# Kernel tuning notes

Measured on AMD Instinct MI355X. Metric: run time of the kernel, lower is better.

The kernel has to match this reference:

```python
import jax, jax.numpy as jnp
import numpy as np

PATCH = 16
FMAP = 14  # 224 // 16, feature-map / mask resolution
BLUR_K = np.array([[1., 2., 1.], [2., 4., 2.], [1., 2., 1.]], dtype=np.float32) / 16.0  # pascal(3), normalized


def _conv(x, w, stride, pad):
    return jax.lax.conv_general_dilated(
        x, w, (stride, stride), [(pad, pad), (pad, pad)],
        dimension_numbers=("NCHW", "OIHW", "NCHW"))


def _max_blur_pool(x):
    # MaxBlurPool2D(kernel_size=3, stride=2, max_pool_size=2, ceil_mode=False):
    x = jax.lax.reduce_window(x, -jnp.inf, jax.lax.max,
                              (1, 1, 2, 2), (1, 1, 1, 1), "VALID")
    C = x.shape[1]
    kw = jnp.broadcast_to(jnp.asarray(BLUR_K, x.dtype), (C, 1, 3, 3))
    return jax.lax.conv_general_dilated(
        x, kw, (2, 2), [(1, 1), (1, 1)],
        dimension_numbers=("NCHW", "OIHW", "NCHW"), feature_group_count=C)


def _up(m, hw):
    # upsample [B,1,FMAP,FMAP] mask to spatial size hw via repeat_interleave
    f = hw // FMAP
    return jnp.repeat(jnp.repeat(m, f, axis=2), f, axis=3)


def reference(x, masks, w1, w2):
    B = x.shape[0]
    m = masks.reshape(B, 1, FMAP, FMAP).astype(x.dtype)  # fmap-level active mask
    x = x * _up(m, x.shape[2])                 # _apply_masks: zero masked 16x16 patches
    x = _conv(x, w1, 2, 3)                     # B,64,112,112
    x = jax.nn.relu(x * _up(m, x.shape[2]))    # SparK-style sparse conv: re-mask output
    x = _max_blur_pool(x)                      # B,64,56,56
    x = _conv(x, w2, 2, 3)                     # B,768,28,28
    x = jax.nn.relu(x * _up(m, x.shape[2]))    # re-mask output of second sparse conv
    x = _max_blur_pool(x)                      # B,768,14,14
    B_, C, H, W = x.shape
    return x.reshape(B_, C, H * W).transpose(0, 2, 1)  # b (h w) c -> [B,196,768]


def setup_inputs() -> dict:
    key = jax.random.key(0)
    k1, k2, k3, k4 = jax.random.split(key, 4)
    x = jax.random.normal(k1, (64, 3, 224, 224), jnp.float32)
    masks = jax.random.randint(k2, (64, 196), 0, 2).astype(bool)
    # kaiming_normal fan_in scaling as in init_weight
    w1 = jax.random.normal(k3, (64, 3, 7, 7), jnp.float32) * np.float32(np.sqrt(2.0 / (3 * 49)))
    w2 = jax.random.normal(k4, (768, 64, 7, 7), jnp.float32) * np.float32(np.sqrt(2.0 / (64 * 49)))
    return {"x": x, "masks": masks, "w1": w1, "w2": w2}
```

## Files before the change

### kernel.cpp

```cpp
#include <hip/hip_runtime.h>
#include <stdint.h>

typedef __attribute__((ext_vector_type(8))) short short8;
typedef __attribute__((ext_vector_type(4))) float f32x4;

#define DEVFN static __device__ __forceinline__

DEVFN float bf2f(uint16_t u) { union { uint32_t i; float f; } v; v.i = ((uint32_t)u) << 16; return v.f; }
DEVFN uint16_t f2bf(float f) {
  union { float f; uint32_t i; } v; v.f = f;
  uint32_t u = v.i;
  u += 0x7fffu + ((u >> 16) & 1u);
  return (uint16_t)(u >> 16);
}
DEVFN int imin(int a, int b) { return a < b ? a : b; }

DEVFN void gl_lds16(const void* g, void* l) {
  __builtin_amdgcn_global_load_lds(
      (__attribute__((address_space(1))) void*)(void*)g,
      (__attribute__((address_space(3))) void*)l, 16, 0, 0);
}

DEVFN f32x4 mfma16(short8 a, short8 b, f32x4 c) {
  return __builtin_amdgcn_mfma_f32_16x16x32_bf16(a, b, c, 0, 0, 0);
}

static constexpr size_t OFF_XP   = 0;
static constexpr size_t OFF_W1T  = 27557888;
static constexpr size_t OFF_W2T  = 27586560;
static constexpr size_t OFF_Y1   = 32403456;
static constexpr size_t OFF_P1   = 135163904;
static constexpr size_t OFF_Y2   = 166653952;
static constexpr size_t OFF_LIST = 243724288;
static constexpr size_t OFF_CNT  = 243774464;
static constexpr size_t WS_NEED  = 243774664;

__global__ __launch_bounds__(256) void k_count(const int* __restrict__ masks, int* __restrict__ cnts) {
  int b = blockIdx.x;
  int gid = b * 256 + threadIdx.x;
  unsigned long long m = __ballot(masks[gid] != 0);
  __shared__ int wsum[4];
  if ((threadIdx.x & 63) == 0) wsum[threadIdx.x >> 6] = __popcll(m);
  __syncthreads();
  if (threadIdx.x == 0) cnts[b] = wsum[0] + wsum[1] + wsum[2] + wsum[3];
}

__global__ __launch_bounds__(256) void k_emit(const int* __restrict__ masks, const int* __restrict__ cnts,
                                              int* __restrict__ list, int* __restrict__ total) {
  int b = blockIdx.x;
  int gid = b * 256 + threadIdx.x;
  int lane = threadIdx.x & 63, wave = threadIdx.x >> 6;
  int base = 0;
  for (int i = 0; i < b; ++i) base += cnts[i];
  bool f = masks[gid] != 0;
  unsigned long long m = __ballot(f);
  __shared__ int wcnt[4];
  if (lane == 0) wcnt[wave] = __popcll(m);
  __syncthreads();
  int woff = 0;
  for (int i = 0; i < wave; ++i) woff += wcnt[i];
  if (f) list[base + woff + __popcll(m & ((1ull << lane) - 1ull))] = gid;
  if (b == 48 && threadIdx.x == 0)
    *total = base + wcnt[0] + wcnt[1] + wcnt[2] + wcnt[3];
}

__global__ __launch_bounds__(256) void k_prep(const float* __restrict__ x, const int* __restrict__ masks,
                                              uint16_t* __restrict__ xp) {
  int gid = blockIdx.x * 256 + threadIdx.x;
  int b = gid / 53824;
  int rc = gid - b * 53824;
  int r2 = rc / 232;
  int c2 = rc - r2 * 232;
  int r = r2 - 3, c = c2 - 3;
  uint16_t o0 = 0, o1 = 0, o2 = 0;
  if ((unsigned)r < 224u && (unsigned)c < 224u) {
    if (masks[b * 196 + (r >> 4) * 14 + (c >> 4)]) {
      const float* px = x + (((size_t)b * 3) * 224 + r) * 224 + c;
      o0 = f2bf(px[0]);
      o1 = f2bf(px[50176]);
      o2 = f2bf(px[100352]);
    }
  }
  ushort4 o; o.x = o0; o.y = o1; o.z = o2; o.w = 0;
  *(ushort4*)(xp + (size_t)gid * 4) = o;
}

__global__ __launch_bounds__(256) void k_wt(const float* __restrict__ w1, const float* __restrict__ w2,
                                            uint16_t* __restrict__ w1t, uint16_t* __restrict__ w2t) {
  int gid = blockIdx.x * 256 + threadIdx.x;
  if (gid < 14336) {
    int kh = gid / 2048; int r = gid - kh * 2048;
    int oc = r >> 5, slot = r & 31;
    int kw = slot >> 2, ic = slot & 3;
    float v = 0.f;
    if (kw < 7 && ic < 3) v = w1[((oc * 3 + ic) * 7 + kh) * 7 + kw];
    w1t[gid] = f2bf(v);
  } else {
    int g2 = gid - 14336;
    int khw = g2 / 49152; int r = g2 - khw * 49152;
    int oc = r >> 6, ic = r & 63;
    int kh = khw / 7, kw = khw - kh * 7;
    w2t[g2] = f2bf(w2[((oc * 64 + ic) * 7 + kh) * 7 + kw]);
  }
}

__global__ __launch_bounds__(256, 3) void k_conv1(const uint16_t* __restrict__ xp, const uint16_t* __restrict__ w1t,
                                                  const int* __restrict__ list, const int* __restrict__ count,
                                                  uint16_t* __restrict__ y1) {
  __shared__ uint16_t sB[7 * 64 * 32];
  __shared__ int sc[2];

  int cnt = *count;
  int blk = blockIdx.x;
  if (blk * 2 >= cnt) return;
  int tid = threadIdx.x, lane = tid & 63, wave = tid >> 6;
  int csw = (lane & 3) ^ ((lane >> 2) & 3);

  {
    const char* wg = (const char*)w1t;
    char* wl = (char*)sB;
#pragma unroll
    for (int t = 0; t < 7; ++t) {
      int ldsoff = t * 4096 + wave * 1024;
      int goff = t * 4096 + (wave * 16 + (lane >> 2)) * 64 + csw * 16;
      gl_lds16(wg + goff, wl + ldsoff);
    }
  }
  if (tid < 2) sc[tid] = list[imin(blk * 2 + tid, cnt - 1)];
  __syncthreads();

  int wm = wave * 32, mrow = lane & 15, kg = lane >> 4;

  const uint16_t* baseA[2];
#pragma unroll
  for (int i = 0; i < 2; ++i) {
    int row = wm + 16 * i + mrow;
    int cell = sc[row >> 6];
    int b = cell / 196, cc = cell - b * 196;
    int ci = cc / 14, cj = cc - ci * 14;
    int p = row & 63;
    int oh = ci * 8 + (p >> 3), ow = cj * 8 + (p & 7);
    baseA[i] = xp + (((size_t)(b * 232 + 2 * oh)) * 232 + 2 * ow) * 4 + kg * 8;
  }
  int ksw = (kg ^ (mrow & 3)) * 8;

  f32x4 acc[2][4];
#pragma unroll
  for (int i = 0; i < 2; ++i)
#pragma unroll
    for (int j = 0; j < 4; ++j) acc[i][j] = f32x4{0.f, 0.f, 0.f, 0.f};

#pragma unroll
  for (int kh = 0; kh < 7; ++kh) {
    short8 a0 = *(const short8*)(baseA[0] + kh * 928);
    short8 a1 = *(const short8*)(baseA[1] + kh * 928);
    const uint16_t* Bk = sB + kh * 2048;
#pragma unroll
    for (int j = 0; j < 4; ++j) {
      short8 bj = *(const short8*)(Bk + (16 * j + mrow) * 32 + ksw);
      acc[0][j] = mfma16(a0, bj, acc[0][j]);
      acc[1][j] = mfma16(a1, bj, acc[1][j]);
    }
  }

#pragma unroll
  for (int i = 0; i < 2; ++i) {
    int rbase = wm + 16 * i;
    int cellidx = blk * 2 + (rbase >> 6);
    if (cellidx >= cnt) continue;
    int cell = sc[rbase >> 6];
    int b = cell / 196, cc = cell - b * 196;
    int ci = cc / 14, cj = cc - ci * 14;
#pragma unroll
    for (int j = 0; j < 4; ++j) {
      int oc = 16 * j + mrow;
#pragma unroll
      for (int r = 0; r < 4; ++r) {
        int row = rbase + kg * 4 + r;
        int p = row & 63;
        int oh = ci * 8 + (p >> 3), ow = cj * 8 + (p & 7);
        float v = acc[i][j][r];
        v = v > 0.f ? v : 0.f;
        y1[(((size_t)(b * 112 + oh)) * 112 + ow) * 64 + oc] = f2bf(v);
      }
    }
  }
}

__global__ __launch_bounds__(256) void k_pool1(const uint16_t* __restrict__ y1, const int* __restrict__ masks,
                                               uint16_t* __restrict__ p1) {
  __shared__ uint16_t sY[18 * 18 * 64];
  int b = blockIdx.y;
  int tile = blockIdx.x;
  int tr = tile >> 3, tc = tile & 7;
  int pr0 = tr * 8, pc0 = tc * 8;
  int R0 = 2 * pr0 - 7, C0 = 2 * pc0 - 7;
  int tid = threadIdx.x;
  const int* mb = masks + b * 196;

  for (int idx = tid; idx < 2592; idx += 256) {
    int pix = idx >> 3, ch = idx & 7;
    int pr = pix / 18, pc = pix - pr * 18;
    int r = R0 + pr, c = C0 + pc;
    short8 v = {0, 0, 0, 0, 0, 0, 0, 0};
    if ((unsigned)r < 112u && (unsigned)c < 112u && mb[(r >> 3) * 14 + (c >> 3)])
      v = *(const short8*)(y1 + (((size_t)(b * 112 + r)) * 112 + c) * 64 + ch * 8);
    *(short8*)(sY + ((size_t)(pr * 18 + pc)) * 64 + ch * 8) = v;
  }
  __syncthreads();

  for (int it = tid; it < 512; it += 256) {
    int opix = it >> 3, ch = it & 7;
    int lr = opix >> 3, lc = opix & 7;
    int pr = pr0 + lr, pc = pc0 + lc;
    if (pr >= 62 || pc >= 62) continue;
    int oh = pr - 3, ow = pc - 3;
    float acc[8] = {0.f, 0.f, 0.f, 0.f, 0.f, 0.f, 0.f, 0.f};
    if ((unsigned)oh < 56u && (unsigned)ow < 56u) {
      float hm_prev[3][8];
#pragma unroll
      for (int dd = 0; dd < 4; ++dd) {
        float yv[4][8];
        const uint16_t* src = sY + ((size_t)((2 * lr + dd) * 18 + 2 * lc)) * 64 + ch * 8;
#pragma unroll
        for (int e = 0; e < 4; ++e) {
          short8 t8 = *(const short8*)(src + e * 64);
#pragma unroll
          for (int k = 0; k < 8; ++k) yv[e][k] = bf2f((uint16_t)t8[k]);
        }
        float hm[3][8];
#pragma unroll
        for (int e = 0; e < 3; ++e) {
          int qc = 2 * ow - 1 + e;
          float cv = ((unsigned)qc <= 110u) ? 1.f : 0.f;
#pragma unroll
          for (int k = 0; k < 8; ++k) hm[e][k] = cv * fmaxf(yv[e][k], yv[e + 1][k]);
        }
        if (dd > 0) {
          int d = dd - 1;
          int qr = 2 * oh - 1 + d;
          if ((unsigned)qr <= 110u) {
            float wd = (d == 1) ? 2.f : 1.f;
#pragma unroll
            for (int e = 0; e < 3; ++e) {
              float w = wd * ((e == 1) ? 2.f : 1.f);
#pragma unroll
              for (int k = 0; k < 8; ++k) acc[k] += w * fmaxf(hm_prev[e][k], hm[e][k]);
            }
          }
        }
#pragma unroll
        for (int e = 0; e < 3; ++e)
#pragma unroll
          for (int k = 0; k < 8; ++k) hm_prev[e][k] = hm[e][k];
      }
#pragma unroll
      for (int k = 0; k < 8; ++k) acc[k] *= (1.f / 16.f);
    }
    short8 o;
#pragma unroll
    for (int k = 0; k < 8; ++k) o[k] = (short)f2bf(acc[k]);
    *(short8*)(p1 + (((size_t)(b * 62 + pr)) * 62 + pc) * 64 + ch * 8) = o;
  }
}

__global__ __launch_bounds__(512, 4) void k_conv2(const uint16_t* __restrict__ p1, const uint16_t* __restrict__ w2t,
                                                  const int* __restrict__ list, const int* __restrict__ count,
                                                  uint16_t* __restrict__ y2) {
  __shared__ uint16_t sA[256 * 64];
  __shared__ uint16_t sBt[128 * 64];

  int cnt = *count;
  int gx = blockIdx.x;
  int xcd = gx & 7, s = gx >> 3;
  int y = s % 6, mtl = s / 6;
  int mt = xcd + 8 * mtl;
  if (mt * 64 >= cnt) return;
  int ocb = y * 128;
  int tid = threadIdx.x, lane = tid & 63, wave = tid >> 6;
  int csw = (lane & 7) ^ ((lane >> 3) & 7);

  int* scs = (int*)sA;
  if (tid < 64) scs[tid] = list[imin(mt * 64 + tid, cnt - 1)];
  __syncthreads();
  int qm = wave & 3, qn = wave >> 2;
  int mrow = lane & 15, kg = lane >> 4;
  int cellA[4], cellE[4];
#pragma unroll
  for (int t = 0; t < 4; ++t) cellA[t] = scs[wave * 8 + t * 2 + (lane >> 5)];
#pragma unroll
  for (int i = 0; i < 4; ++i) cellE[i] = scs[qm * 16 + 4 * i + kg];
  __syncthreads();

  const char* gA[4];
#pragma unroll
  for (int t = 0; t < 4; ++t) {
    int r = wave * 32 + t * 8 + (lane >> 3);
    int cell = cellA[t];
    int b = cell / 196, cc = cell - b * 196;
    int ci = cc / 14, cj = cc - ci * 14;
    int p = r & 3;
    int oh = 2 * ci + (p >> 1), ow = 2 * cj + (p & 1);
    gA[t] = (const char*)p1 + (((size_t)(b * 62 + 2 * oh)) * 62 + 2 * ow) * 128 + csw * 16;
  }
  const char* gB[2];
#pragma unroll
  for (int t = 0; t < 2; ++t) {
    int oc = ocb + wave * 16 + t * 8 + (lane >> 3);
    gB[t] = (const char*)w2t + (size_t)oc * 128 + csw * 16;
  }

  f32x4 acc[4][4];
#pragma unroll
  for (int i = 0; i < 4; ++i)
#pragma unroll
    for (int j = 0; j < 4; ++j) acc[i][j] = f32x4{0.f, 0.f, 0.f, 0.f};

  int sw = mrow & 7;
  int kh = 0, kw = 0;

#pragma unroll 1
  for (int it = 0; it < 49; ++it) {
    size_t offA = (size_t)(kh * 62 + kw) * 128;
    size_t offB = (size_t)it * 98304;
    char* la = (char*)sA + (wave * 32) * 128;
    char* lb = (char*)sBt + (wave * 16) * 128;
#pragma unroll
    for (int t = 0; t < 4; ++t) gl_lds16(gA[t] + offA, la + t * 1024);
#pragma unroll
    for (int t = 0; t < 2; ++t) gl_lds16(gB[t] + offB, lb + t * 1024);
    __syncthreads();
#pragma unroll
    for (int ks = 0; ks < 2; ++ks) {
      int koff = ((ks * 4 + kg) ^ sw) * 8;
      short8 a[4], bb[4];
#pragma unroll
      for (int i = 0; i < 4; ++i)
        a[i] = *(const short8*)(sA + (qm * 64 + 16 * i + mrow) * 64 + koff);
#pragma unroll
      for (int j = 0; j < 4; ++j)
        bb[j] = *(const short8*)(sBt + (qn * 64 + 16 * j + mrow) * 64 + koff);
#pragma unroll
      for (int i = 0; i < 4; ++i)
#pragma unroll
        for (int j = 0; j < 4; ++j)
          acc[i][j] = mfma16(a[i], bb[j], acc[i][j]);
    }
    __syncthreads();
    if (++kw == 7) { kw = 0; ++kh; }
  }

#pragma unroll
  for (int i = 0; i < 4; ++i) {
    int cellslot = qm * 16 + 4 * i + kg;
    int cellidx = mt * 64 + cellslot;
    if (cellidx >= cnt) continue;
    int cell = cellE[i];
    int b = cell / 196, cc = cell - b * 196;
    int ci = cc / 14, cj = cc - ci * 14;
#pragma unroll
    for (int j = 0; j < 4; ++j) {
      int oc = ocb + qn * 64 + 16 * j + mrow;
#pragma unroll
      for (int r = 0; r < 4; ++r) {
        int oh = 2 * ci + (r >> 1), ow = 2 * cj + (r & 1);
        float v = acc[i][j][r];
        v = v > 0.f ? v : 0.f;
        y2[(((size_t)(b * 784)) + oh * 28 + ow) * 768 + oc] = f2bf(v);
      }
    }
  }
}

__global__ __launch_bounds__(256) void k_pool2(const uint16_t* __restrict__ y2, const int* __restrict__ masks,
                                               float* __restrict__ out) {
  __shared__ uint16_t sY[4 * 28 * 128];
  int chunk = blockIdx.x, pi = blockIdx.y, b = blockIdx.z;
  int ch0 = chunk * 128;
  int tid = threadIdx.x;
  const int* mb = masks + b * 196;

  for (int idx = tid; idx < 1792; idx += 256) {
    int rc = idx >> 4;
    int sub = idx & 15;
    int k = rc / 28, c = rc - k * 28;
    int r = 2 * pi - 1 + k;
    short8 v = {0, 0, 0, 0, 0, 0, 0, 0};
    if ((unsigned)r < 28u && mb[(r >> 1) * 14 + (c >> 1)])
      v = *(const short8*)(y2 + (((size_t)(b * 784)) + r * 28 + c) * 768 + ch0 + sub * 8);
    *(short8*)(sY + ((size_t)(k * 28 + c)) * 128 + sub * 8) = v;
  }
  __syncthreads();

  for (int idx = tid; idx < 1792; idx += 256) {
    int pj = idx >> 7, ch = idx & 127;
    float v[4][4];
#pragma unroll
    for (int e = 0; e < 4; ++e) {
      int col = 2 * pj - 1 + e;
      bool cv = (unsigned)col < 28u;
#pragma unroll
      for (int k = 0; k < 4; ++k)
        v[k][e] = cv ? bf2f(sY[((size_t)(k * 28 + col)) * 128 + ch]) : 0.f;
    }
    float acc = 0.f;
#pragma unroll
    for (int d = 0; d < 3; ++d) {
      int q = 2 * pi - 1 + d;
      float gd = ((unsigned)q <= 26u) ? ((d == 1) ? 2.f : 1.f) : 0.f;
      float s = 0.f;
#pragma unroll
      for (int e = 0; e < 3; ++e) {
        int q2 = 2 * pj - 1 + e;
        float ge = ((unsigned)q2 <= 26u) ? ((e == 1) ? 2.f : 1.f) : 0.f;
        float m = fmaxf(fmaxf(v[d][e], v[d + 1][e]), fmaxf(v[d][e + 1], v[d + 1][e + 1]));
        s += ge * m;
      }
      acc += gd * s;
    }
    out[(((size_t)(b * 196)) + pi * 14 + pj) * 768 + ch0 + ch] = acc * (1.f / 16.f);
  }
}

extern "C" void kernel_launch(void* const* d_in, const int* in_sizes, int n_in,
                              void* d_out, int out_size, void* d_ws, size_t ws_size,
                              hipStream_t stream) {
  const float* x     = (const float*)d_in[0];
  const int*   masks = (const int*)d_in[1];
  const float* w1    = (const float*)d_in[2];
  const float* w2    = (const float*)d_in[3];

  char* ws = (char*)d_ws;
  if (ws_size < WS_NEED) return;

  uint16_t* xp  = (uint16_t*)(ws + OFF_XP);
  uint16_t* w1t = (uint16_t*)(ws + OFF_W1T);
  uint16_t* w2t = (uint16_t*)(ws + OFF_W2T);
  uint16_t* y1  = (uint16_t*)(ws + OFF_Y1);
  uint16_t* p1  = (uint16_t*)(ws + OFF_P1);
  uint16_t* y2  = (uint16_t*)(ws + OFF_Y2);
  int* list     = (int*)(ws + OFF_LIST);
  int* cnts     = (int*)(ws + OFF_CNT);
  int* total    = cnts + 49;

  k_count<<<49, 256, 0, stream>>>(masks, cnts);
  k_emit<<<49, 256, 0, stream>>>(masks, cnts, list, total);
  k_prep<<<13456, 256, 0, stream>>>(x, masks, xp);
  k_wt<<<9464, 256, 0, stream>>>(w1, w2, w1t, w2t);
  k_conv1<<<6272, 256, 0, stream>>>(xp, w1t, list, total, y1);
  k_pool1<<<dim3(64, 64), 256, 0, stream>>>(y1, masks, p1);
  k_conv2<<<1200, 512, 0, stream>>>(p1, w2t, list, total, y2);
  k_pool2<<<dim3(6, 14, 64), 256, 0, stream>>>(y2, masks, (float*)d_out);
}
```

Measured before the change: 382.6 us.

## Double-buffer conv2 LDS tiles to overlap global loads with MFMA

Moves the conv2 LDS tiles to 96 KB of dynamic shared memory, split into two A/B buffers, and prefetches the next filter tap while MFMAs run on the current one. Raw s_waitcnt and s_barrier calls replace __syncthreads, and s_setprio is raised around the MFMA block. The goal is to hide global-to-LDS load latency that the old single-buffer loop exposed on every tap. In exchange, the larger LDS footprint and the launch bound cut from 4 to 2 lower the number of resident blocks.

```diff
diff --git a/kernel.cpp b/kernel.cpp
--- a/kernel.cpp
+++ b/kernel.cpp
@@ -264,11 +264,14 @@
   }
 }
 
-__global__ __launch_bounds__(512, 4) void k_conv2(const uint16_t* __restrict__ p1, const uint16_t* __restrict__ w2t,
+__global__ __launch_bounds__(512, 2) void k_conv2(const uint16_t* __restrict__ p1, const uint16_t* __restrict__ w2t,
                                                   const int* __restrict__ list, const int* __restrict__ count,
                                                   uint16_t* __restrict__ y2) {
-  __shared__ uint16_t sA[256 * 64];
-  __shared__ uint16_t sBt[128 * 64];
+  extern __shared__ uint16_t smem[];
+  uint16_t* sA0 = smem;
+  uint16_t* sA1 = smem + 16384;
+  uint16_t* sB0 = smem + 32768;
+  uint16_t* sB1 = smem + 40960;
 
   int cnt = *count;
   int gx = blockIdx.x;
@@ -280,7 +283,7 @@
   int tid = threadIdx.x, lane = tid & 63, wave = tid >> 6;
   int csw = (lane & 7) ^ ((lane >> 3) & 7);
 
-  int* scs = (int*)sA;
+  int* scs = (int*)smem;
   if (tid < 64) scs[tid] = list[imin(mt * 64 + tid, cnt - 1)];
   __syncthreads();
   int qm = wave & 3, qn = wave >> 2;
@@ -316,39 +319,76 @@
 #pragma unroll
     for (int j = 0; j < 4; ++j) acc[i][j] = f32x4{0.f, 0.f, 0.f, 0.f};
 
-  int sw = mrow & 7;
-  int kh = 0, kw = 0;
+  int sw8 = mrow & 7;
+  int ko0 = (kg ^ sw8) * 8;
+  int ko1 = ((4 + kg) ^ sw8) * 8;
+  const int arow = (qm * 64 + mrow) * 64;
+  const int brow = (qn * 64 + mrow) * 64;
+
+  char* laA0 = (char*)sA0 + (wave * 32) * 128;
+  char* laA1 = (char*)sA1 + (wave * 32) * 128;
+  char* laB0 = (char*)sB0 + (wave * 16) * 128;
+  char* laB1 = (char*)sB1 + (wave * 16) * 128;
+
+#pragma unroll
+  for (int t = 0; t < 4; ++t) gl_lds16(gA[t], laA0 + t * 1024);
+#pragma unroll
+  for (int t = 0; t < 2; ++t) gl_lds16(gB[t], laB0 + t * 1024);
+#pragma unroll
+  for (int t = 0; t < 4; ++t) gl_lds16(gA[t] + 128, laA1 + t * 1024);
+#pragma unroll
+  for (int t = 0; t < 2; ++t) gl_lds16(gB[t] + 98304, laB1 + t * 1024);
+  asm volatile("s_waitcnt vmcnt(6)" ::: "memory");
+  __builtin_amdgcn_s_barrier();
+  __builtin_amdgcn_sched_barrier(0);
+
+  int kws = 2, khs = 0;
+
+#define CONV2_BODY(bufA, bufB, laA, laB, T)                                   \
+  {                                                                           \
+    short8 a0_[4], b0_[4], a1_[4], b1_[4];                                    \
+    _Pragma("unroll") for (int i = 0; i < 4; ++i)                             \
+      a0_[i] = *(const short8*)((bufA) + arow + i * 1024 + ko0);              \
+    _Pragma("unroll") for (int j = 0; j < 4; ++j)                             \
+      b0_[j] = *(const short8*)((bufB) + brow + j * 1024 + ko0);              \
+    _Pragma("unroll") for (int i = 0; i < 4; ++i)                             \
+      a1_[i] = *(const short8*)((bufA) + arow + i * 1024 + ko1);              \
+    _Pragma("unroll") for (int j = 0; j < 4; ++j)                             \
+      b1_[j] = *(const short8*)((bufB) + brow + j * 1024 + ko1);              \
+    __builtin_amdgcn_s_setprio(1);                                            \
+    _Pragma("unroll") for (int i = 0; i < 4; ++i)                             \
+      _Pragma("unroll") for (int j = 0; j < 4; ++j)                           \
+        acc[i][j] = mfma16(a0_[i], b0_[j], acc[i][j]);                        \
+    _Pragma("unroll") for (int i = 0; i < 4; ++i)                             \
+      _Pragma("unroll") for (int j = 0; j < 4; ++j)                           \
+        acc[i][j] = mfma16(a1_[i], b1_[j], acc[i][j]);                        \
+    __builtin_amdgcn_s_setprio(0);                                            \
+    asm volatile("s_waitcnt lgkmcnt(0)" ::: "memory");                        \
+    __builtin_amdgcn_sched_barrier(0);                                        \
+    __builtin_amdgcn_s_barrier();       \
+    __builtin_amdgcn_sched_barrier(0);                                        \
+    if ((T) < 47) {                                                           \
+      size_t offA_ = (size_t)(khs * 62 + kws) * 128;                          \
+      size_t offB_ = (size_t)((T) + 2) * 98304;                               \
+      _Pragma("unroll") for (int t_ = 0; t_ < 4; ++t_)                        \
+        gl_lds16(gA[t_] + offA_, (laA) + t_ * 1024);                          \
+      _Pragma("unroll") for (int t_ = 0; t_ < 2; ++t_)                        \
+        gl_lds16(gB[t_] + offB_, (laB) + t_ * 1024);                          \
+      if (++kws == 7) { kws = 0; ++khs; }                                     \
+      asm volatile("s_waitcnt vmcnt(6)" ::: "memory");    \
+    } else {                                                                  \
+      asm volatile("s_waitcnt vmcnt(0)" ::: "memory");                        \
+    }                                                                         \
+    __builtin_amdgcn_s_barrier();              \
+    __builtin_amdgcn_sched_barrier(0);                                        \
+  }
 
 #pragma unroll 1
-  for (int it = 0; it < 49; ++it) {
-    size_t offA = (size_t)(kh * 62 + kw) * 128;
-    size_t offB = (size_t)it * 98304;
-    char* la = (char*)sA + (wave * 32) * 128;
-    char* lb = (char*)sBt + (wave * 16) * 128;
-#pragma unroll
-    for (int t = 0; t < 4; ++t) gl_lds16(gA[t] + offA, la + t * 1024);
-#pragma unroll
-    for (int t = 0; t < 2; ++t) gl_lds16(gB[t] + offB, lb + t * 1024);
-    __syncthreads();
-#pragma unroll
-    for (int ks = 0; ks < 2; ++ks) {
-      int koff = ((ks * 4 + kg) ^ sw) * 8;
-      short8 a[4], bb[4];
-#pragma unroll
-      for (int i = 0; i < 4; ++i)
-        a[i] = *(const short8*)(sA + (qm * 64 + 16 * i + mrow) * 64 + koff);
-#pragma unroll
-      for (int j = 0; j < 4; ++j)
-        bb[j] = *(const short8*)(sBt + (qn * 64 + 16 * j + mrow) * 64 + koff);
-#pragma unroll
-      for (int i = 0; i < 4; ++i)
-#pragma unroll
-        for (int j = 0; j < 4; ++j)
-          acc[i][j] = mfma16(a[i], bb[j], acc[i][j]);
-    }
-    __syncthreads();
-    if (++kw == 7) { kw = 0; ++kh; }
-  }
+  for (int t = 0; t < 49; t += 2) {
+    CONV2_BODY(sA0, sB0, laA0, laB0, t);
+    if (t + 1 < 49) CONV2_BODY(sA1, sB1, laA1, laB1, t + 1);
+  }
+#undef CONV2_BODY
 
 #pragma unroll
   for (int i = 0; i < 4; ++i) {
@@ -443,12 +483,19 @@
   int* cnts     = (int*)(ws + OFF_CNT);
   int* total    = cnts + 49;
 
+  static int conv2_attr_done = 0;
+  if (!conv2_attr_done) {
+    (void)hipFuncSetAttribute((const void*)k_conv2,
+                              hipFuncAttributeMaxDynamicSharedMemorySize, 98304);
+    conv2_attr_done = 1;
+  }
+
   k_count<<<49, 256, 0, stream>>>(masks, cnts);
   k_emit<<<49, 256, 0, stream>>>(masks, cnts, list, total);
   k_prep<<<13456, 256, 0, stream>>>(x, masks, xp);
   k_wt<<<9464, 256, 0, stream>>>(w1, w2, w1t, w2t);
   k_conv1<<<6272, 256, 0, stream>>>(xp, w1t, list, total, y1);
   k_pool1<<<dim3(64, 64), 256, 0, stream>>>(y1, masks, p1);
-  k_conv2<<<1200, 512, 0, stream>>>(p1, w2t, list, total, y2);
+  k_conv2<<<1200, 512, 98304, stream>>>(p1, w2t, list, total, y2);
   k_pool2<<<dim3(6, 14, 64), 256, 0, stream>>>(y2, masks, (float*)d_out);
 }
```

Result: slower. 410.1 us (+7.2%).

## Double-buffer conv2 weight tiles in LDS and load activations directly from global

Applied to the files above, without the earlier changes.

The conv2 implicit-GEMM loop now keeps only the weight tile in LDS, double-buffered so the next tap's weights are prefetched while the current tap's MFMAs run, with one barrier per iteration instead of two. Activation fragments are read straight from global memory into registers per wave, dropping the A-tile LDS staging. MFMA sections are wrapped in setprio hints. The trade-off is that activation loads become uncoalesced per-lane global reads, duplicated across the two qn waves, and their latency is exposed directly before the MFMAs.

```diff
diff --git a/kernel.cpp b/kernel.cpp
--- a/kernel.cpp
+++ b/kernel.cpp
@@ -267,8 +267,8 @@
 __global__ __launch_bounds__(512, 4) void k_conv2(const uint16_t* __restrict__ p1, const uint16_t* __restrict__ w2t,
                                                   const int* __restrict__ list, const int* __restrict__ count,
                                                   uint16_t* __restrict__ y2) {
-  __shared__ uint16_t sA[256 * 64];
-  __shared__ uint16_t sBt[128 * 64];
+  __shared__ uint16_t sB[2][128 * 64];
+  __shared__ int scs[64];
 
   int cnt = *count;
   int gx = blockIdx.x;
@@ -280,35 +280,32 @@
   int tid = threadIdx.x, lane = tid & 63, wave = tid >> 6;
   int csw = (lane & 7) ^ ((lane >> 3) & 7);
 
-  int* scs = (int*)sA;
   if (tid < 64) scs[tid] = list[imin(mt * 64 + tid, cnt - 1)];
   __syncthreads();
+
   int qm = wave & 3, qn = wave >> 2;
   int mrow = lane & 15, kg = lane >> 4;
-  int cellA[4], cellE[4];
-#pragma unroll
-  for (int t = 0; t < 4; ++t) cellA[t] = scs[wave * 8 + t * 2 + (lane >> 5)];
-#pragma unroll
-  for (int i = 0; i < 4; ++i) cellE[i] = scs[qm * 16 + 4 * i + kg];
-  __syncthreads();
-
-  const char* gA[4];
-#pragma unroll
-  for (int t = 0; t < 4; ++t) {
-    int r = wave * 32 + t * 8 + (lane >> 3);
-    int cell = cellA[t];
+
+  uint32_t ofsA[4];
+#pragma unroll
+  for (int i = 0; i < 4; ++i) {
+    int cell = scs[qm * 16 + 4 * i + (mrow >> 2)];
     int b = cell / 196, cc = cell - b * 196;
     int ci = cc / 14, cj = cc - ci * 14;
-    int p = r & 3;
+    int p = mrow & 3;
     int oh = 2 * ci + (p >> 1), ow = 2 * cj + (p & 1);
-    gA[t] = (const char*)p1 + (((size_t)(b * 62 + 2 * oh)) * 62 + 2 * ow) * 128 + csw * 16;
-  }
-  const char* gB[2];
-#pragma unroll
-  for (int t = 0; t < 2; ++t) {
-    int oc = ocb + wave * 16 + t * 8 + (lane >> 3);
-    gB[t] = (const char*)w2t + (size_t)oc * 128 + csw * 16;
-  }
+    ofsA[i] = (uint32_t)(((b * 62 + 2 * oh) * 62 + 2 * ow) * 128) + (uint32_t)(kg * 16);
+  }
+  uint32_t ofsB0, ofsB1;
+  {
+    int oc0 = ocb + wave * 16 + (lane >> 3);
+    int oc1 = oc0 + 8;
+    ofsB0 = (uint32_t)(oc0 * 128 + csw * 16);
+    ofsB1 = (uint32_t)(oc1 * 128 + csw * 16);
+  }
+  int sw8 = mrow & 7;
+  const char* p1c = (const char*)p1;
+  const char* w2c = (const char*)w2t;
 
   f32x4 acc[4][4];
 #pragma unroll
@@ -316,37 +313,58 @@
 #pragma unroll
     for (int j = 0; j < 4; ++j) acc[i][j] = f32x4{0.f, 0.f, 0.f, 0.f};
 
-  int sw = mrow & 7;
+  {
+    char* lb = (char*)sB[0] + wave * 2048;
+    gl_lds16(w2c + ofsB0, lb);
+    gl_lds16(w2c + ofsB1, lb + 1024);
+  }
+  __syncthreads();
+
+  const uint16_t* sBc = sB[0];
+  uint16_t* sBn = sB[1];
   int kh = 0, kw = 0;
+  int ko0 = (kg ^ sw8) * 8;
+  int ko1 = ((4 + kg) ^ sw8) * 8;
 
 #pragma unroll 1
-  for (int it = 0; it < 49; ++it) {
-    size_t offA = (size_t)(kh * 62 + kw) * 128;
-    size_t offB = (size_t)it * 98304;
-    char* la = (char*)sA + (wave * 32) * 128;
-    char* lb = (char*)sBt + (wave * 16) * 128;
-#pragma unroll
-    for (int t = 0; t < 4; ++t) gl_lds16(gA[t] + offA, la + t * 1024);
-#pragma unroll
-    for (int t = 0; t < 2; ++t) gl_lds16(gB[t] + offB, lb + t * 1024);
-    __syncthreads();
-#pragma unroll
-    for (int ks = 0; ks < 2; ++ks) {
-      int koff = ((ks * 4 + kg) ^ sw) * 8;
-      short8 a[4], bb[4];
-#pragma unroll
-      for (int i = 0; i < 4; ++i)
-        a[i] = *(const short8*)(sA + (qm * 64 + 16 * i + mrow) * 64 + koff);
-#pragma unroll
-      for (int j = 0; j < 4; ++j)
-        bb[j] = *(const short8*)(sBt + (qn * 64 + 16 * j + mrow) * 64 + koff);
-#pragma unroll
-      for (int i = 0; i < 4; ++i)
-#pragma unroll
-        for (int j = 0; j < 4; ++j)
-          acc[i][j] = mfma16(a[i], bb[j], acc[i][j]);
-    }
-    __syncthreads();
+  for (int t = 0; t < 49; ++t) {
+    if (t < 48) {
+      uint32_t offB = (uint32_t)(t + 1) * 98304u;
+      char* lb = (char*)sBn + wave * 2048;
+      gl_lds16(w2c + (size_t)(offB + ofsB0), lb);
+      gl_lds16(w2c + (size_t)(offB + ofsB1), lb + 1024);
+    }
+    uint32_t offA = (uint32_t)((kh * 62 + kw) * 128);
+    short8 a0[4];
+#pragma unroll
+    for (int i = 0; i < 4; ++i) a0[i] = *(const short8*)(p1c + (size_t)(ofsA[i] + offA));
+    short8 bb[4];
+#pragma unroll
+    for (int j = 0; j < 4; ++j)
+      bb[j] = *(const short8*)(sBc + (qn * 64 + 16 * j + mrow) * 64 + ko0);
+    __builtin_amdgcn_s_setprio(1);
+#pragma unroll
+    for (int i = 0; i < 4; ++i)
+#pragma unroll
+      for (int j = 0; j < 4; ++j) acc[i][j] = mfma16(a0[i], bb[j], acc[i][j]);
+    __builtin_amdgcn_s_setprio(0);
+    short8 a1[4];
+#pragma unroll
+    for (int i = 0; i < 4; ++i) a1[i] = *(const short8*)(p1c + (size_t)(ofsA[i] + offA + 64));
+#pragma unroll
+    for (int j = 0; j < 4; ++j)
+      bb[j] = *(const short8*)(sBc + (qn * 64 + 16 * j + mrow) * 64 + ko1);
+    __builtin_amdgcn_s_setprio(1);
+#pragma unroll
+    for (int i = 0; i < 4; ++i)
+#pragma unroll
+      for (int j = 0; j < 4; ++j) acc[i][j] = mfma16(a1[i], bb[j], acc[i][j]);
+    __builtin_amdgcn_s_setprio(0);
+    asm volatile("s_waitcnt vmcnt(0)" ::: "memory");
+    __builtin_amdgcn_sched_barrier(0);
+    __builtin_amdgcn_s_barrier();
+    __builtin_amdgcn_sched_barrier(0);
+    const uint16_t* tmp = sBc; sBc = sBn; sBn = (uint16_t*)tmp;
     if (++kw == 7) { kw = 0; ++kh; }
   }
 
@@ -355,7 +373,7 @@
     int cellslot = qm * 16 + 4 * i + kg;
     int cellidx = mt * 64 + cellslot;
     if (cellidx >= cnt) continue;
-    int cell = cellE[i];
+    int cell = scs[cellslot];
     int b = cell / 196, cc = cell - b * 196;
     int ci = cc / 14, cj = cc - ci * 14;
 #pragma unroll
```

New measurement: 539.8 us. +41.1%, slower.
